# Kernel optimization log

Hardware: AMD Instinct MI355X
Metric: run time of the kernel (lower is better)

Reference implementation:

```python
import jax, jax.numpy as jnp
import numpy as np

N = 100000
E = 1600000
IN_C, HID, HEADS, OUT_C = 128, 32, 4, 32
NEG_SLOPE = 0.2


def gat_layer(x, edge_index, W, att_src, att_dst, bias, concat):
    """PyG-style GATConv: h = xW, per-edge attention, segment softmax over dst, scatter-add."""
    n = x.shape[0]
    H, C = att_src.shape
    h = (x @ W).reshape(n, H, C)                      # [N, H, C]
    src, dst = edge_index[0], edge_index[1]
    a_s = jnp.sum(h * att_src, axis=-1)               # [N, H]
    a_d = jnp.sum(h * att_dst, axis=-1)               # [N, H]
    e = jax.nn.leaky_relu(a_s[src] + a_d[dst], NEG_SLOPE)   # [E, H]
    # numerically stable segment softmax over incoming edges of each dst node
    m = jax.ops.segment_max(e, dst, num_segments=n)   # [N, H]
    ex = jnp.exp(e - m[dst])
    denom = jax.ops.segment_sum(ex, dst, num_segments=n)
    alpha = ex / denom[dst]                           # [E, H]
    msg = h[src] * alpha[:, :, None]                  # [E, H, C]
    out = jax.ops.segment_sum(msg, dst, num_segments=n)  # [N, H, C]
    out = out.reshape(n, H * C) if concat else out.mean(axis=1)
    return out + bias


def add_self_loops(edge_index, n):
    ar = jnp.arange(n, dtype=edge_index.dtype)
    loops = jnp.stack([ar, ar])
    return jnp.concatenate([edge_index, loops], axis=1)


def setup_inputs() -> dict:
    key = jax.random.key(0)
    ks = jax.random.split(key, 10)
    x = jax.random.normal(ks[0], (N, IN_C), dtype=jnp.float32)
    edge_index = jax.random.randint(ks[1], (2, E), 0, N, dtype=jnp.int64)
    s = 0.1
    W1 = jax.random.normal(ks[2], (IN_C, HEADS * HID), dtype=jnp.float32) * s
    att_src1 = jax.random.normal(ks[3], (HEADS, HID), dtype=jnp.float32) * s
    att_dst1 = jax.random.normal(ks[4], (HEADS, HID), dtype=jnp.float32) * s
    b1 = jnp.zeros((HEADS * HID,), dtype=jnp.float32)
    W2 = jax.random.normal(ks[5], (HEADS * HID, OUT_C), dtype=jnp.float32) * s
    att_src2 = jax.random.normal(ks[6], (1, OUT_C), dtype=jnp.float32) * s
    att_dst2 = jax.random.normal(ks[7], (1, OUT_C), dtype=jnp.float32) * s
    b2 = jnp.zeros((OUT_C,), dtype=jnp.float32)
    return {"x": x, "edge_index": edge_index,
            "W1": W1, "att_src1": att_src1, "att_dst1": att_dst1, "b1": b1,
            "W2": W2, "att_src2": att_src2, "att_dst2": att_dst2, "b2": b2}


def reference(x, edge_index, W1, att_src1, att_dst1, b1, W2, att_src2, att_dst2, b2):
    ei = add_self_loops(edge_index, x.shape[0])
    h = gat_layer(x, ei, W1, att_src1, att_dst1, b1, concat=True)
    h = jax.nn.elu(h)
    h = gat_layer(h, ei, W2, att_src2, att_dst2, b2, concat=False)
    return jax.nn.log_softmax(h, axis=1)
```

## Files before the change

### kernel.cpp

```cpp
#include <hip/hip_runtime.h>
#include <hip/hip_fp16.h>
#include <math.h>

#define IN_C   128
#define HEADS  4
#define F1     128
#define OUT_C  32
#define NEG    0.2f
#define SH     8
#define CHA    8192
#define SCB    4096

__device__ __forceinline__ unsigned short f2h(float f) {
    return __half_as_ushort(__float2half_rn(f));
}
__device__ __forceinline__ float h2f(unsigned short u) {
    return __half2float(__ushort_as_half(u));
}
__device__ __forceinline__ float hlo(unsigned u) { return h2f((unsigned short)(u & 0xffffu)); }
__device__ __forceinline__ float hhi(unsigned u) { return h2f((unsigned short)(u >> 16)); }
__device__ __forceinline__ unsigned pk2(float a, float b) {
    return (unsigned)f2h(a) | ((unsigned)f2h(b) << 16);
}
typedef _Float16 h2v __attribute__((ext_vector_type(2)));
__device__ __forceinline__ h2v u2h2(unsigned u) {
    h2v r; __builtin_memcpy(&r, &u, 4); return r;
}
__device__ __forceinline__ float dot2(unsigned a, unsigned b, float c) {
    return __builtin_amdgcn_fdot2(u2h2(a), u2h2(b), c, false);
}
#define PERM_LO 0x05040100u
#define PERM_HI 0x07060302u
__device__ __forceinline__ float pdot(unsigned b, unsigned a, unsigned sel, h2v pv, float c) {
    return __builtin_amdgcn_fdot2(u2h2(__builtin_amdgcn_perm(b, a, sel)), pv, c, false);
}

__global__ __launch_bounds__(256) void k_bhist(
    const int* __restrict__ ei, int* __restrict__ bmat, int E_, int n, int NB, int NC)
{
    __shared__ int h[512];
    int t = threadIdx.x, c = blockIdx.x;
    for (int i = t; i < NB; i += 256) h[i] = 0;
    __syncthreads();
    int e0 = c * CHA, e1 = min(e0 + CHA, E_ + n);
    for (int e = e0 + t; e < e1; e += 256) {
        int d = (e < E_) ? ei[E_ + e] : e - E_;
        atomicAdd(&h[d >> SH], 1);
    }
    __syncthreads();
    for (int i = t; i < NB; i += 256) bmat[i * NC + c] = h[i];
}

__global__ __launch_bounds__(256) void k_scanA(
    int* __restrict__ bmat, int* __restrict__ bsums, int M)
{
    __shared__ int sm[256];
    int t = threadIdx.x;
    int base = blockIdx.x * SCB + t * 16;
    int v[16];
    int s = 0;
    #pragma unroll
    for (int j = 0; j < 16; ++j) {
        int i = base + j;
        v[j] = (i < M) ? bmat[i] : 0;
        s += v[j];
    }
    sm[t] = s;
    __syncthreads();
    for (int off = 1; off < 256; off <<= 1) {
        int a = (t >= off) ? sm[t - off] : 0;
        __syncthreads();
        sm[t] += a;
        __syncthreads();
    }
    int excl = sm[t] - s;
    #pragma unroll
    for (int j = 0; j < 16; ++j) {
        int i = base + j;
        if (i < M) bmat[i] = excl;
        excl += v[j];
    }
    if (t == 255) bsums[blockIdx.x] = sm[255];
}

__global__ __launch_bounds__(256) void k_scanB(int* __restrict__ bsums, int NBLK)
{
    __shared__ int sm[256];
    int t = threadIdx.x;
    int v = (t < NBLK) ? bsums[t] : 0;
    sm[t] = v;
    __syncthreads();
    for (int off = 1; off < 256; off <<= 1) {
        int a = (t >= off) ? sm[t - off] : 0;
        __syncthreads();
        sm[t] += a;
        __syncthreads();
    }
    if (t < NBLK) bsums[t] = sm[t] - v;
}

__global__ __launch_bounds__(256) void k_scanC(
    int* __restrict__ bmat, const int* __restrict__ bsums, int M)
{
    int i = blockIdx.x * 256 + threadIdx.x;
    if (i < M) bmat[i] += bsums[i >> 12];
}

__global__ __launch_bounds__(256) void k_bscatter(
    const int* __restrict__ ei, const int* __restrict__ bmat,
    unsigned* __restrict__ recs, int E_, int n, int NB, int NC)
{
    __shared__ int cur[512];
    int t = threadIdx.x, c = blockIdx.x;
    for (int i = t; i < NB; i += 256) cur[i] = bmat[i * NC + c];
    __syncthreads();
    int e0 = c * CHA, e1 = min(e0 + CHA, E_ + n);
    for (int e = e0 + t; e < e1; e += 256) {
        int s, d;
        if (e < E_) { s = ei[e]; d = ei[E_ + e]; } else { s = d = e - E_; }
        int b = d >> SH;
        int p = atomicAdd(&cur[b], 1);
        recs[p] = ((unsigned)(d & ((1 << SH) - 1)) << 17) | (unsigned)s;
    }
}

__global__ __launch_bounds__(256) void k_bfill(
    const unsigned* __restrict__ recs, const int* __restrict__ bmat,
    int* __restrict__ row_off, int* __restrict__ csr, int n, int NB, int NC, int EE)
{
    __shared__ int deg[256];
    __shared__ int cur[256];
    int t = threadIdx.x, b = blockIdx.x;
    int r0 = bmat[b * NC];
    int r1 = (b + 1 < NB) ? bmat[(b + 1) * NC] : EE;
    deg[t] = 0;
    __syncthreads();
    for (int i = r0 + t; i < r1; i += 256)
        atomicAdd(&deg[recs[i] >> 17], 1);
    __syncthreads();
    int v = deg[t];
    for (int off = 1; off < 256; off <<= 1) {
        int a = (t >= off) ? deg[t - off] : 0;
        __syncthreads();
        deg[t] += a;
        __syncthreads();
    }
    int excl = deg[t] - v;
    int dst = (b << SH) + t;
    if (dst < n) row_off[dst] = r0 + excl;
    cur[t] = excl;
    if (b == NB - 1 && t == 0) row_off[n] = EE;
    __syncthreads();
    for (int i = r0 + t; i < r1; i += 256) {
        unsigned rec = recs[i];
        int dl = rec >> 17;
        int p = atomicAdd(&cur[dl], 1);
        csr[r0 + p] = (int)(rec & 0x1FFFFu);
    }
}

__global__ __launch_bounds__(256) void k_gemm1(
    const float* __restrict__ x, const float* __restrict__ W,
    const float* __restrict__ as_w, const float* __restrict__ ad_w,
    unsigned short* __restrict__ h1h, float* __restrict__ as1,
    float* __restrict__ ad1, int n)
{
    __shared__ unsigned Ws2[64 * 64];
    __shared__ unsigned xs2[64 * 64];
    int t = threadIdx.x;
    int half = blockIdx.x & 1;
    int n0 = (blockIdx.x >> 1) * 64;

    for (int i = t; i < 64 * 16; i += 256) {
        int k2 = i >> 4, c4 = (i & 15) * 4;
        const float* w0 = &W[(2 * k2) * 128 + half * 64 + c4];
        const float* w1 = &W[(2 * k2 + 1) * 128 + half * 64 + c4];
        float4 a = *(const float4*)w0;
        float4 b = *(const float4*)w1;
        uint4 p;
        p.x = pk2(a.x, b.x); p.y = pk2(a.y, b.y);
        p.z = pk2(a.z, b.z); p.w = pk2(a.w, b.w);
        *(uint4*)&Ws2[k2 * 64 + c4] = p;
    }
    for (int i = t; i < 64 * 32; i += 256) {
        int nl = i & 63, k4 = (i >> 6) * 4;
        int nn = n0 + nl;
        float4 v = (nn < n) ? *(const float4*)&x[(size_t)nn * 128 + k4]
                            : make_float4(0.f, 0.f, 0.f, 0.f);
        xs2[(k4 >> 1) * 64 + nl]       = pk2(v.x, v.y);
        xs2[((k4 >> 1) + 1) * 64 + nl] = pk2(v.z, v.w);
    }
    __syncthreads();

    int tx = t & 15, ty = t >> 4;
    float acc[4][4] = {};
    #pragma unroll 4
    for (int k2 = 0; k2 < 64; ++k2) {
        uint4 a = *(uint4*)&xs2[k2 * 64 + ty * 4];
        uint4 b = *(uint4*)&Ws2[k2 * 64 + tx * 4];
        unsigned av[4] = {a.x, a.y, a.z, a.w};
        unsigned bv[4] = {b.x, b.y, b.z, b.w};
        #pragma unroll
        for (int i = 0; i < 4; ++i)
            #pragma unroll
            for (int j = 0; j < 4; ++j)
                acc[i][j] = dot2(av[i], bv[j], acc[i][j]);
    }
    int cbase = half * 64 + tx * 4;
    float4 aws = *(const float4*)&as_w[cbase];
    float4 awd = *(const float4*)&ad_w[cbase];
    float sa[4], sd[4];
    #pragma unroll
    for (int i = 0; i < 4; ++i) {
        int nn = n0 + ty * 4 + i;
        sa[i] = acc[i][0]*aws.x + acc[i][1]*aws.y + acc[i][2]*aws.z + acc[i][3]*aws.w;
        sd[i] = acc[i][0]*awd.x + acc[i][1]*awd.y + acc[i][2]*awd.z + acc[i][3]*awd.w;
        if (nn < n) {
            ushort4 p;
            p.x = f2h(acc[i][0]); p.y = f2h(acc[i][1]);
            p.z = f2h(acc[i][2]); p.w = f2h(acc[i][3]);
            *(ushort4*)&h1h[(size_t)nn * 128 + cbase] = p;
        }
    }
    #pragma unroll
    for (int o = 1; o < 8; o <<= 1) {
        #pragma unroll
        for (int i = 0; i < 4; ++i) {
            sa[i] += __shfl_xor(sa[i], o);
            sd[i] += __shfl_xor(sd[i], o);
        }
    }
    if ((tx & 7) == 0) {
        int head = half * 2 + (tx >> 3);
        #pragma unroll
        for (int i = 0; i < 4; ++i) {
            int nn = n0 + ty * 4 + i;
            if (nn < n) {
                as1[(size_t)nn * 4 + head] = sa[i];
                ad1[(size_t)nn * 4 + head] = sd[i];
            }
        }
    }
}

__global__ __launch_bounds__(256) void k_gemm2(
    const float* __restrict__ z, const float* __restrict__ W,
    const float* __restrict__ as_w, const float* __restrict__ ad_w,
    unsigned short* __restrict__ h2h, float* __restrict__ as2,
    float* __restrict__ ad2, int n)
{
    __shared__ unsigned Ws2[64 * 32];
    __shared__ unsigned zs2[64 * 64];
    int t = threadIdx.x;
    int n0 = blockIdx.x * 64;

    for (int i = t; i < 64 * 8; i += 256) {
        int k2 = i >> 3, c4 = (i & 7) * 4;
        float4 a = *(const float4*)&W[(2 * k2) * 32 + c4];
        float4 b = *(const float4*)&W[(2 * k2 + 1) * 32 + c4];
        uint4 p;
        p.x = pk2(a.x, b.x); p.y = pk2(a.y, b.y);
        p.z = pk2(a.z, b.z); p.w = pk2(a.w, b.w);
        *(uint4*)&Ws2[k2 * 32 + c4] = p;
    }
    for (int i = t; i < 64 * 32; i += 256) {
        int nl = i & 63, k4 = (i >> 6) * 4;
        int nn = n0 + nl;
        float4 v = (nn < n) ? *(const float4*)&z[(size_t)nn * 128 + k4]
                            : make_float4(0.f, 0.f, 0.f, 0.f);
        zs2[(k4 >> 1) * 64 + nl]       = pk2(v.x, v.y);
        zs2[((k4 >> 1) + 1) * 64 + nl] = pk2(v.z, v.w);
    }
    __syncthreads();

    int tx = t & 7, ty = t >> 3;
    float acc[2][4] = {};
    #pragma unroll 4
    for (int k2 = 0; k2 < 64; ++k2) {
        uint2 a = *(uint2*)&zs2[k2 * 64 + ty * 2];
        uint4 b = *(uint4*)&Ws2[k2 * 32 + tx * 4];
        unsigned av[2] = {a.x, a.y};
        unsigned bv[4] = {b.x, b.y, b.z, b.w};
        #pragma unroll
        for (int i = 0; i < 2; ++i)
            #pragma unroll
            for (int j = 0; j < 4; ++j)
                acc[i][j] = dot2(av[i], bv[j], acc[i][j]);
    }
    float4 aws = *(const float4*)&as_w[tx * 4];
    float4 awd = *(const float4*)&ad_w[tx * 4];
    float sa[2], sd[2];
    #pragma unroll
    for (int i = 0; i < 2; ++i) {
        int nn = n0 + ty * 2 + i;
        sa[i] = acc[i][0]*aws.x + acc[i][1]*aws.y + acc[i][2]*aws.z + acc[i][3]*aws.w;
        sd[i] = acc[i][0]*awd.x + acc[i][1]*awd.y + acc[i][2]*awd.z + acc[i][3]*awd.w;
        if (nn < n) {
            ushort4 p;
            p.x = f2h(acc[i][0]); p.y = f2h(acc[i][1]);
            p.z = f2h(acc[i][2]); p.w = f2h(acc[i][3]);
            *(ushort4*)&h2h[(size_t)nn * 32 + tx * 4] = p;
        }
    }
    #pragma unroll
    for (int o = 1; o < 8; o <<= 1) {
        #pragma unroll
        for (int i = 0; i < 2; ++i) {
            sa[i] += __shfl_xor(sa[i], o);
            sd[i] += __shfl_xor(sd[i], o);
        }
    }
    if (tx == 0) {
        #pragma unroll
        for (int i = 0; i < 2; ++i) {
            int nn = n0 + ty * 2 + i;
            if (nn < n) { as2[nn] = sa[i]; ad2[nn] = sd[i]; }
        }
    }
}

__global__ __launch_bounds__(256) void k_gat1(
    const int* __restrict__ row_off, const int* __restrict__ csr,
    const float* __restrict__ as1, const float* __restrict__ ad1,
    const unsigned short* __restrict__ h1h, const float* __restrict__ b1,
    float* __restrict__ z, int n)
{
    int nb = threadIdx.x >> 4;
    int hl = threadIdx.x & 15;
    int node = blockIdx.x * 16 + nb;
    if (node >= n) return;
    __shared__ int            s_src[16][16];
    __shared__ unsigned short s_p16[16][4][16];
    int* ssrc = s_src[nb];
    unsigned short (*sp16)[16] = s_p16[nb];

    const char* h1b = (const char*)h1h;
    int chb  = hl << 4;
    int head = hl >> 2;

    float4 addv = *(const float4*)&ad1[(size_t)node * 4];
    int beg = row_off[node], end = row_off[node + 1];

    float sr0 = 0.f, sr1 = 0.f, sr2 = 0.f, sr3 = 0.f;
    float acc0 = 0.f, acc1 = 0.f, acc2 = 0.f, acc3 = 0.f;
    float acc4 = 0.f, acc5 = 0.f, acc6 = 0.f, acc7 = 0.f;

    for (int c = beg; c < end; c += 16) {
        int cnt = min(16, end - c);
        bool has = hl < cnt;
        float ls0 = 0.f, ls1 = 0.f, ls2 = 0.f, ls3 = 0.f;
        if (has) {
            int sA = csr[c + hl];
            ssrc[hl] = sA << 8;
            float4 av = *(const float4*)(as1 + ((unsigned)sA << 2));
            float v;
            v = av.x + addv.x; v = v > 0.f ? v : NEG * v; v = fminf(v, 10.f);
            unsigned short q0 = f2h(__expf(v));
            v = av.y + addv.y; v = v > 0.f ? v : NEG * v; v = fminf(v, 10.f);
            unsigned short q1 = f2h(__expf(v));
            v = av.z + addv.z; v = v > 0.f ? v : NEG * v; v = fminf(v, 10.f);
            unsigned short q2 = f2h(__expf(v));
            v = av.w + addv.w; v = v > 0.f ? v : NEG * v; v = fminf(v, 10.f);
            unsigned short q3 = f2h(__expf(v));
            sp16[0][hl] = q0; sp16[1][hl] = q1;
            sp16[2][hl] = q2; sp16[3][hl] = q3;
            ls0 = h2f(q0); ls1 = h2f(q1); ls2 = h2f(q2); ls3 = h2f(q3);
        }
        #pragma unroll
        for (int o = 8; o; o >>= 1) {
            ls0 += __shfl_xor(ls0, o);
            ls1 += __shfl_xor(ls1, o);
            ls2 += __shfl_xor(ls2, o);
            ls3 += __shfl_xor(ls3, o);
        }
        sr0 += ls0; sr1 += ls1; sr2 += ls2; sr3 += ls3;
        __threadfence_block();

        #define PAIR1(j) {                                                    \
            int2 oo = *(const int2*)&ssrc[j];                                 \
            unsigned pp = *(const unsigned*)&sp16[head][j];                   \
            uint4 A = *(const uint4*)(h1b + (unsigned)(oo.x + chb));          \
            uint4 B = *(const uint4*)(h1b + (unsigned)(oo.y + chb));          \
            h2v pv = u2h2(pp);                                                \
            acc0 = pdot(B.x, A.x, PERM_LO, pv, acc0);                         \
            acc1 = pdot(B.x, A.x, PERM_HI, pv, acc1);                         \
            acc2 = pdot(B.y, A.y, PERM_LO, pv, acc2);                         \
            acc3 = pdot(B.y, A.y, PERM_HI, pv, acc3);                         \
            acc4 = pdot(B.z, A.z, PERM_LO, pv, acc4);                         \
            acc5 = pdot(B.z, A.z, PERM_HI, pv, acc5);                         \
            acc6 = pdot(B.w, A.w, PERM_LO, pv, acc6);                         \
            acc7 = pdot(B.w, A.w, PERM_HI, pv, acc7);                         \
        }
        int jj = 0;
        for (; jj + 4 <= cnt; jj += 4) {
            PAIR1(jj);
            PAIR1(jj + 2);
        }
        if (jj + 2 <= cnt) {
            PAIR1(jj);
            jj += 2;
        }
        if (jj < cnt) {
            int o0 = ssrc[jj];
            float p = h2f(sp16[head][jj]);
            uint4 A = *(const uint4*)(h1b + (unsigned)(o0 + chb));
            acc0 = fmaf(p, hlo(A.x), acc0);
            acc1 = fmaf(p, hhi(A.x), acc1);
            acc2 = fmaf(p, hlo(A.y), acc2);
            acc3 = fmaf(p, hhi(A.y), acc3);
            acc4 = fmaf(p, hlo(A.z), acc4);
            acc5 = fmaf(p, hhi(A.z), acc5);
            acc6 = fmaf(p, hlo(A.w), acc6);
            acc7 = fmaf(p, hhi(A.w), acc7);
        }
        #undef PAIR1
    }
    float srh = head == 0 ? sr0 : head == 1 ? sr1 : head == 2 ? sr2 : sr3;
    float inv = 1.0f / srh;
    float4 bb0 = *(const float4*)&b1[hl * 8];
    float4 bb1 = *(const float4*)&b1[hl * 8 + 4];
    float v0 = acc0 * inv + bb0.x;
    float v1 = acc1 * inv + bb0.y;
    float v2 = acc2 * inv + bb0.z;
    float v3 = acc3 * inv + bb0.w;
    float v4 = acc4 * inv + bb1.x;
    float v5 = acc5 * inv + bb1.y;
    float v6 = acc6 * inv + bb1.z;
    float v7 = acc7 * inv + bb1.w;
    v0 = v0 > 0.f ? v0 : (__expf(v0) - 1.f);
    v1 = v1 > 0.f ? v1 : (__expf(v1) - 1.f);
    v2 = v2 > 0.f ? v2 : (__expf(v2) - 1.f);
    v3 = v3 > 0.f ? v3 : (__expf(v3) - 1.f);
    v4 = v4 > 0.f ? v4 : (__expf(v4) - 1.f);
    v5 = v5 > 0.f ? v5 : (__expf(v5) - 1.f);
    v6 = v6 > 0.f ? v6 : (__expf(v6) - 1.f);
    v7 = v7 > 0.f ? v7 : (__expf(v7) - 1.f);
    float* zr = &z[(size_t)node * F1 + hl * 8];
    *(float4*)zr       = make_float4(v0, v1, v2, v3);
    *(float4*)(zr + 4) = make_float4(v4, v5, v6, v7);
}

__global__ __launch_bounds__(256) void k_gat2(
    const int* __restrict__ row_off, const int* __restrict__ csr,
    const float* __restrict__ as2, const float* __restrict__ ad2,
    const unsigned short* __restrict__ h2h, const float* __restrict__ b2,
    float* __restrict__ y, int n)
{
    int nb = threadIdx.x >> 2;
    int hl = threadIdx.x & 3;
    int node = blockIdx.x * 64 + nb;
    if (node >= n) return;
    __shared__ int            s_src[64][34];
    __shared__ unsigned short s_p16[64][34];
    int* ssrc = s_src[nb];
    unsigned short* sp16 = s_p16[nb];

    const char* h2b = (const char*)h2h;
    int chb = hl << 4;

    float addv = ad2[node];
    int beg = row_off[node], end = row_off[node + 1];
    float sr = 0.f;
    float acc0 = 0.f, acc1 = 0.f, acc2 = 0.f, acc3 = 0.f;
    float acc4 = 0.f, acc5 = 0.f, acc6 = 0.f, acc7 = 0.f;

    for (int c = beg; c < end; c += 32) {
        int cnt = min(32, end - c);
        int e0 = hl << 3;
        float ls = 0.f;
        #pragma unroll
        for (int k = 0; k < 8; k += 2) {
            int e = e0 + k;
            if (e < cnt) {
                unsigned short qa, qb = 0;
                int sA = csr[c + e];
                ssrc[e] = sA << 6;
                float v = as2[(unsigned)sA] + addv;
                v = v > 0.f ? v : NEG * v;
                qa = f2h(__expf(fminf(v, 10.f)));
                if (e + 1 < cnt) {
                    int sB = csr[c + e + 1];
                    ssrc[e + 1] = sB << 6;
                    float w2 = as2[(unsigned)sB] + addv;
                    w2 = w2 > 0.f ? w2 : NEG * w2;
                    qb = f2h(__expf(fminf(w2, 10.f)));
                }
                *(unsigned*)&sp16[e] = (unsigned)qa | ((unsigned)qb << 16);
                ls += h2f(qa) + h2f(qb);
            }
        }
        ls += __shfl_xor(ls, 1);
        ls += __shfl_xor(ls, 2);
        sr += ls;
        __threadfence_block();

        #define PAIR2(j) {                                                    \
            int2 oo = *(const int2*)&ssrc[j];                                 \
            unsigned pp = *(const unsigned*)&sp16[j];                         \
            uint4 A = *(const uint4*)(h2b + (unsigned)(oo.x + chb));          \
            uint4 B = *(const uint4*)(h2b + (unsigned)(oo.y + chb));          \
            h2v pv = u2h2(pp);                                                \
            acc0 = pdot(B.x, A.x, PERM_LO, pv, acc0);                         \
            acc1 = pdot(B.x, A.x, PERM_HI, pv, acc1);                         \
            acc2 = pdot(B.y, A.y, PERM_LO, pv, acc2);                         \
            acc3 = pdot(B.y, A.y, PERM_HI, pv, acc3);                         \
            acc4 = pdot(B.z, A.z, PERM_LO, pv, acc4);                         \
            acc5 = pdot(B.z, A.z, PERM_HI, pv, acc5);                         \
            acc6 = pdot(B.w, A.w, PERM_LO, pv, acc6);                         \
            acc7 = pdot(B.w, A.w, PERM_HI, pv, acc7);                         \
        }
        int jj = 0;
        for (; jj + 4 <= cnt; jj += 4) {
            PAIR2(jj);
            PAIR2(jj + 2);
        }
        if (jj + 2 <= cnt) {
            PAIR2(jj);
            jj += 2;
        }
        if (jj < cnt) {
            int o0 = ssrc[jj];
            float p = h2f(sp16[jj]);
            uint4 A = *(const uint4*)(h2b + (unsigned)(o0 + chb));
            acc0 = fmaf(p, hlo(A.x), acc0);
            acc1 = fmaf(p, hhi(A.x), acc1);
            acc2 = fmaf(p, hlo(A.y), acc2);
            acc3 = fmaf(p, hhi(A.y), acc3);
            acc4 = fmaf(p, hlo(A.z), acc4);
            acc5 = fmaf(p, hhi(A.z), acc5);
            acc6 = fmaf(p, hlo(A.w), acc6);
            acc7 = fmaf(p, hhi(A.w), acc7);
        }
        #undef PAIR2
    }
    float inv = 1.0f / sr;
    float4 bb0 = *(const float4*)&b2[hl * 8];
    float4 bb1 = *(const float4*)&b2[hl * 8 + 4];
    float v0 = acc0 * inv + bb0.x;
    float v1 = acc1 * inv + bb0.y;
    float v2 = acc2 * inv + bb0.z;
    float v3 = acc3 * inv + bb0.w;
    float v4 = acc4 * inv + bb1.x;
    float v5 = acc5 * inv + bb1.y;
    float v6 = acc6 * inv + bb1.z;
    float v7 = acc7 * inv + bb1.w;
    float m = fmaxf(fmaxf(fmaxf(v0, v1), fmaxf(v2, v3)),
                    fmaxf(fmaxf(v4, v5), fmaxf(v6, v7)));
    m = fmaxf(m, __shfl_xor(m, 1));
    m = fmaxf(m, __shfl_xor(m, 2));
    float ss = __expf(v0 - m) + __expf(v1 - m) + __expf(v2 - m) + __expf(v3 - m)
             + __expf(v4 - m) + __expf(v5 - m) + __expf(v6 - m) + __expf(v7 - m);
    ss += __shfl_xor(ss, 1);
    ss += __shfl_xor(ss, 2);
    float lg = m + logf(ss);
    float* yr = &y[(size_t)node * OUT_C + hl * 8];
    *(float4*)yr       = make_float4(v0 - lg, v1 - lg, v2 - lg, v3 - lg);
    *(float4*)(yr + 4) = make_float4(v4 - lg, v5 - lg, v6 - lg, v7 - lg);
}

extern "C" void kernel_launch(void* const* d_in, const int* in_sizes, int n_in,
                              void* d_out, int out_size, void* d_ws, size_t ws_size,
                              hipStream_t stream) {
    const float* x    = (const float*)d_in[0];
    const int*   ei   = (const int*)d_in[1];
    const float* W1   = (const float*)d_in[2];
    const float* as1w = (const float*)d_in[3];
    const float* ad1w = (const float*)d_in[4];
    const float* b1   = (const float*)d_in[5];
    const float* W2   = (const float*)d_in[6];
    const float* as2w = (const float*)d_in[7];
    const float* ad2w = (const float*)d_in[8];
    const float* b2   = (const float*)d_in[9];
    float* out = (float*)d_out;

    int n  = in_sizes[0] / IN_C;
    int E_ = in_sizes[1] / 2;
    int EE = E_ + n;

    int NB = (n + (1 << SH) - 1) >> SH;
    int NC = (EE + CHA - 1) / CHA;
    int M  = NB * NC;
    int NBLK = (M + SCB - 1) / SCB;

    char* w = (char*)d_ws;
    size_t off = 0;
    auto take = [&](size_t elems) { void* p = w + off; off += ((elems * 4 + 255) & ~(size_t)255); return p; };
    int* bmat      = (int*)take((size_t)M);
    int* bsums     = (int*)take(256);
    unsigned* recs = (unsigned*)take((size_t)EE);
    int* row_off   = (int*)take((size_t)n + 1);
    int* csr       = (int*)take((size_t)EE);
    float* as1     = (float*)take((size_t)n * 4);
    float* ad1     = (float*)take((size_t)n * 4);
    unsigned short* h1h = (unsigned short*)take((size_t)n * 64);
    float* z       = (float*)take((size_t)n * 128);
    unsigned short* h2h = (unsigned short*)take((size_t)n * 16);
    float* as2     = (float*)take((size_t)n);
    float* ad2     = (float*)take((size_t)n);

    k_bhist   <<<NC, 256, 0, stream>>>(ei, bmat, E_, n, NB, NC);
    k_scanA   <<<NBLK, 256, 0, stream>>>(bmat, bsums, M);
    k_scanB   <<<1, 256, 0, stream>>>(bsums, NBLK);
    k_scanC   <<<(M + 255) / 256, 256, 0, stream>>>(bmat, bsums, M);
    k_bscatter<<<NC, 256, 0, stream>>>(ei, bmat, recs, E_, n, NB, NC);
    k_bfill   <<<NB, 256, 0, stream>>>(recs, bmat, row_off, csr, n, NB, NC, EE);

    int nt = (n + 63) / 64;
    k_gemm1<<<nt * 2, 256, 0, stream>>>(x, W1, as1w, ad1w, h1h, as1, ad1, n);
    int gG = (n + 15) / 16;
    k_gat1<<<gG, 256, 0, stream>>>(row_off, csr, as1, ad1, h1h, b1, z, n);

    k_gemm2<<<nt, 256, 0, stream>>>(z, W2, as2w, ad2w, h2h, as2, ad2, n);
    int gG2 = (n + 63) / 64;
    k_gat2<<<gG2, 256, 0, stream>>>(row_off, csr, as2, ad2, h2h, b2, out, n);
}
```

Measured before the change: 339.3 us.

## Fuse second-layer GEMM into GAT1 aggregation and fold scan fixup into consumers

The layer-2 linear transform and its attention-score dot products now run inside k_gat1. Each node's ELU output is packed to fp16 in shared memory and multiplied by a W2 tile held in LDS, so the 51 MB fp32 z intermediate is never written to or read back from global memory. The separate k_scanC pass is also removed: k_bscatter and k_bfill add the block offsets from bsums when they read bmat. The cost is that every gat1 block reloads and converts W2, plus extra LDS use that may lower occupancy.

```diff
diff --git a/kernel.cpp b/kernel.cpp
--- a/kernel.cpp
+++ b/kernel.cpp
@@ -99,20 +99,18 @@
     if (t < NBLK) bsums[t] = sm[t] - v;
 }
 
-__global__ __launch_bounds__(256) void k_scanC(
-    int* __restrict__ bmat, const int* __restrict__ bsums, int M)
-{
-    int i = blockIdx.x * 256 + threadIdx.x;
-    if (i < M) bmat[i] += bsums[i >> 12];
-}
 
 __global__ __launch_bounds__(256) void k_bscatter(
     const int* __restrict__ ei, const int* __restrict__ bmat,
-    unsigned* __restrict__ recs, int E_, int n, int NB, int NC)
+    const int* __restrict__ bsums, unsigned* __restrict__ recs,
+    int E_, int n, int NB, int NC)
 {
     __shared__ int cur[512];
     int t = threadIdx.x, c = blockIdx.x;
-    for (int i = t; i < NB; i += 256) cur[i] = bmat[i * NC + c];
+    for (int i = t; i < NB; i += 256) {
+        int m = i * NC + c;
+        cur[i] = bmat[m] + bsums[m >> 12];
+    }
     __syncthreads();
     int e0 = c * CHA, e1 = min(e0 + CHA, E_ + n);
     for (int e = e0 + t; e < e1; e += 256) {
@@ -126,13 +124,19 @@
 
 __global__ __launch_bounds__(256) void k_bfill(
     const unsigned* __restrict__ recs, const int* __restrict__ bmat,
-    int* __restrict__ row_off, int* __restrict__ csr, int n, int NB, int NC, int EE)
+    const int* __restrict__ bsums, int* __restrict__ row_off,
+    int* __restrict__ csr, int n, int NB, int NC, int EE)
 {
     __shared__ int deg[256];
     __shared__ int cur[256];
     int t = threadIdx.x, b = blockIdx.x;
-    int r0 = bmat[b * NC];
-    int r1 = (b + 1 < NB) ? bmat[(b + 1) * NC] : EE;
+    int m0 = b * NC;
+    int r0 = bmat[m0] + bsums[m0 >> 12];
+    int r1 = EE;
+    if (b + 1 < NB) {
+        int m1 = (b + 1) * NC;
+        r1 = bmat[m1] + bsums[m1 >> 12];
+    }
     deg[t] = 0;
     __syncthreads();
     for (int i = r0 + t; i < r1; i += 256)
@@ -243,201 +247,167 @@
     }
 }
 
-__global__ __launch_bounds__(256) void k_gemm2(
-    const float* __restrict__ z, const float* __restrict__ W,
-    const float* __restrict__ as_w, const float* __restrict__ ad_w,
-    unsigned short* __restrict__ h2h, float* __restrict__ as2,
-    float* __restrict__ ad2, int n)
-{
-    __shared__ unsigned Ws2[64 * 32];
-    __shared__ unsigned zs2[64 * 64];
-    int t = threadIdx.x;
-    int n0 = blockIdx.x * 64;
-
-    for (int i = t; i < 64 * 8; i += 256) {
-        int k2 = i >> 3, c4 = (i & 7) * 4;
-        float4 a = *(const float4*)&W[(2 * k2) * 32 + c4];
-        float4 b = *(const float4*)&W[(2 * k2 + 1) * 32 + c4];
-        uint4 p;
-        p.x = pk2(a.x, b.x); p.y = pk2(a.y, b.y);
-        p.z = pk2(a.z, b.z); p.w = pk2(a.w, b.w);
-        *(uint4*)&Ws2[k2 * 32 + c4] = p;
-    }
-    for (int i = t; i < 64 * 32; i += 256) {
-        int nl = i & 63, k4 = (i >> 6) * 4;
-        int nn = n0 + nl;
-        float4 v = (nn < n) ? *(const float4*)&z[(size_t)nn * 128 + k4]
-                            : make_float4(0.f, 0.f, 0.f, 0.f);
-        zs2[(k4 >> 1) * 64 + nl]       = pk2(v.x, v.y);
-        zs2[((k4 >> 1) + 1) * 64 + nl] = pk2(v.z, v.w);
-    }
-    __syncthreads();
-
-    int tx = t & 7, ty = t >> 3;
-    float acc[2][4] = {};
-    #pragma unroll 4
-    for (int k2 = 0; k2 < 64; ++k2) {
-        uint2 a = *(uint2*)&zs2[k2 * 64 + ty * 2];
-        uint4 b = *(uint4*)&Ws2[k2 * 32 + tx * 4];
-        unsigned av[2] = {a.x, a.y};
-        unsigned bv[4] = {b.x, b.y, b.z, b.w};
-        #pragma unroll
-        for (int i = 0; i < 2; ++i)
-            #pragma unroll
-            for (int j = 0; j < 4; ++j)
-                acc[i][j] = dot2(av[i], bv[j], acc[i][j]);
-    }
-    float4 aws = *(const float4*)&as_w[tx * 4];
-    float4 awd = *(const float4*)&ad_w[tx * 4];
-    float sa[2], sd[2];
-    #pragma unroll
-    for (int i = 0; i < 2; ++i) {
-        int nn = n0 + ty * 2 + i;
-        sa[i] = acc[i][0]*aws.x + acc[i][1]*aws.y + acc[i][2]*aws.z + acc[i][3]*aws.w;
-        sd[i] = acc[i][0]*awd.x + acc[i][1]*awd.y + acc[i][2]*awd.z + acc[i][3]*awd.w;
-        if (nn < n) {
-            ushort4 p;
-            p.x = f2h(acc[i][0]); p.y = f2h(acc[i][1]);
-            p.z = f2h(acc[i][2]); p.w = f2h(acc[i][3]);
-            *(ushort4*)&h2h[(size_t)nn * 32 + tx * 4] = p;
-        }
-    }
-    #pragma unroll
-    for (int o = 1; o < 8; o <<= 1) {
-        #pragma unroll
-        for (int i = 0; i < 2; ++i) {
-            sa[i] += __shfl_xor(sa[i], o);
-            sd[i] += __shfl_xor(sd[i], o);
-        }
-    }
-    if (tx == 0) {
-        #pragma unroll
-        for (int i = 0; i < 2; ++i) {
-            int nn = n0 + ty * 2 + i;
-            if (nn < n) { as2[nn] = sa[i]; ad2[nn] = sd[i]; }
-        }
-    }
-}
-
 __global__ __launch_bounds__(256) void k_gat1(
     const int* __restrict__ row_off, const int* __restrict__ csr,
     const float* __restrict__ as1, const float* __restrict__ ad1,
     const unsigned short* __restrict__ h1h, const float* __restrict__ b1,
-    float* __restrict__ z, int n)
-{
-    int nb = threadIdx.x >> 4;
-    int hl = threadIdx.x & 15;
-    int node = blockIdx.x * 16 + nb;
-    if (node >= n) return;
+    const float* __restrict__ W2, const float* __restrict__ as2w,
+    const float* __restrict__ ad2w, unsigned short* __restrict__ h2h,
+    float* __restrict__ as2, float* __restrict__ ad2, int n)
+{
     __shared__ int            s_src[16][16];
     __shared__ unsigned short s_p16[16][4][16];
-    int* ssrc = s_src[nb];
-    unsigned short (*sp16)[16] = s_p16[nb];
-
-    const char* h1b = (const char*)h1h;
-    int chb  = hl << 4;
-    int head = hl >> 2;
-
-    float4 addv = *(const float4*)&ad1[(size_t)node * 4];
-    int beg = row_off[node], end = row_off[node + 1];
-
-    float sr0 = 0.f, sr1 = 0.f, sr2 = 0.f, sr3 = 0.f;
-    float acc0 = 0.f, acc1 = 0.f, acc2 = 0.f, acc3 = 0.f;
-    float acc4 = 0.f, acc5 = 0.f, acc6 = 0.f, acc7 = 0.f;
-
-    for (int c = beg; c < end; c += 16) {
-        int cnt = min(16, end - c);
-        bool has = hl < cnt;
-        float ls0 = 0.f, ls1 = 0.f, ls2 = 0.f, ls3 = 0.f;
-        if (has) {
-            int sA = csr[c + hl];
-            ssrc[hl] = sA << 8;
-            float4 av = *(const float4*)(as1 + ((unsigned)sA << 2));
-            float v;
-            v = av.x + addv.x; v = v > 0.f ? v : NEG * v; v = fminf(v, 10.f);
-            unsigned short q0 = f2h(__expf(v));
-            v = av.y + addv.y; v = v > 0.f ? v : NEG * v; v = fminf(v, 10.f);
-            unsigned short q1 = f2h(__expf(v));
-            v = av.z + addv.z; v = v > 0.f ? v : NEG * v; v = fminf(v, 10.f);
-            unsigned short q2 = f2h(__expf(v));
-            v = av.w + addv.w; v = v > 0.f ? v : NEG * v; v = fminf(v, 10.f);
-            unsigned short q3 = f2h(__expf(v));
-            sp16[0][hl] = q0; sp16[1][hl] = q1;
-            sp16[2][hl] = q2; sp16[3][hl] = q3;
-            ls0 = h2f(q0); ls1 = h2f(q1); ls2 = h2f(q2); ls3 = h2f(q3);
-        }
+    __shared__ unsigned       W2s[64 * 32];
+    __shared__ unsigned       zs[16][66];
+    int t = threadIdx.x;
+
+    for (int i = t; i < 64 * 8; i += 256) {
+        int k2 = i >> 3, c4 = (i & 7) * 4;
+        float4 a = *(const float4*)&W2[(2 * k2) * 32 + c4];
+        float4 b = *(const float4*)&W2[(2 * k2 + 1) * 32 + c4];
+        uint4 p;
+        p.x = pk2(a.x, b.x); p.y = pk2(a.y, b.y);
+        p.z = pk2(a.z, b.z); p.w = pk2(a.w, b.w);
+        *(uint4*)&W2s[k2 * 32 + c4] = p;
+    }
+    __syncthreads();
+
+    int nb = t >> 4;
+    int hl = t & 15;
+    int node = blockIdx.x * 16 + nb;
+    if (node < n) {
+        int* ssrc = s_src[nb];
+        unsigned short (*sp16)[16] = s_p16[nb];
+
+        const char* h1b = (const char*)h1h;
+        int chb  = hl << 4;
+        int head = hl >> 2;
+
+        float4 addv = *(const float4*)&ad1[(size_t)node * 4];
+        int beg = row_off[node], end = row_off[node + 1];
+
+        float sr0 = 0.f, sr1 = 0.f, sr2 = 0.f, sr3 = 0.f;
+        float acc0 = 0.f, acc1 = 0.f, acc2 = 0.f, acc3 = 0.f;
+        float acc4 = 0.f, acc5 = 0.f, acc6 = 0.f, acc7 = 0.f;
+
+        for (int c = beg; c < end; c += 16) {
+            int cnt = min(16, end - c);
+            bool has = hl < cnt;
+            float ls0 = 0.f, ls1 = 0.f, ls2 = 0.f, ls3 = 0.f;
+            if (has) {
+                int sA = csr[c + hl];
+                ssrc[hl] = sA << 8;
+                float4 av = *(const float4*)(as1 + ((unsigned)sA << 2));
+                float v;
+                v = av.x + addv.x; v = v > 0.f ? v : NEG * v; v = fminf(v, 10.f);
+                unsigned short q0 = f2h(__expf(v));
+                v = av.y + addv.y; v = v > 0.f ? v : NEG * v; v = fminf(v, 10.f);
+                unsigned short q1 = f2h(__expf(v));
+                v = av.z + addv.z; v = v > 0.f ? v : NEG * v; v = fminf(v, 10.f);
+                unsigned short q2 = f2h(__expf(v));
+                v = av.w + addv.w; v = v > 0.f ? v : NEG * v; v = fminf(v, 10.f);
+                unsigned short q3 = f2h(__expf(v));
+                sp16[0][hl] = q0; sp16[1][hl] = q1;
+                sp16[2][hl] = q2; sp16[3][hl] = q3;
+                ls0 = h2f(q0); ls1 = h2f(q1); ls2 = h2f(q2); ls3 = h2f(q3);
+            }
+            #pragma unroll
+            for (int o = 8; o; o >>= 1) {
+                ls0 += __shfl_xor(ls0, o);
+                ls1 += __shfl_xor(ls1, o);
+                ls2 += __shfl_xor(ls2, o);
+                ls3 += __shfl_xor(ls3, o);
+            }
+            sr0 += ls0; sr1 += ls1; sr2 += ls2; sr3 += ls3;
+            __threadfence_block();
+
+            #define PAIR1(j) {                                                    \
+                int2 oo = *(const int2*)&ssrc[j];                                 \
+                unsigned pp = *(const unsigned*)&sp16[head][j];                   \
+                uint4 A = *(const uint4*)(h1b + (unsigned)(oo.x + chb));          \
+                uint4 B = *(const uint4*)(h1b + (unsigned)(oo.y + chb));          \
+                h2v pv = u2h2(pp);                                                \
+                acc0 = pdot(B.x, A.x, PERM_LO, pv, acc0);                         \
+                acc1 = pdot(B.x, A.x, PERM_HI, pv, acc1);                         \
+                acc2 = pdot(B.y, A.y, PERM_LO, pv, acc2);                         \
+                acc3 = pdot(B.y, A.y, PERM_HI, pv, acc3);                         \
+                acc4 = pdot(B.z, A.z, PERM_LO, pv, acc4);                         \
+                acc5 = pdot(B.z, A.z, PERM_HI, pv, acc5);                         \
+                acc6 = pdot(B.w, A.w, PERM_LO, pv, acc6);                         \
+                acc7 = pdot(B.w, A.w, PERM_HI, pv, acc7);                         \
+            }
+            int jj = 0;
+            for (; jj + 4 <= cnt; jj += 4) {
+                PAIR1(jj);
+                PAIR1(jj + 2);
+            }
+            if (jj + 2 <= cnt) {
+                PAIR1(jj);
+                jj += 2;
+            }
+            if (jj < cnt) {
+                int o0 = ssrc[jj];
+                float p = h2f(sp16[head][jj]);
+                uint4 A = *(const uint4*)(h1b + (unsigned)(o0 + chb));
+                acc0 = fmaf(p, hlo(A.x), acc0);
+                acc1 = fmaf(p, hhi(A.x), acc1);
+                acc2 = fmaf(p, hlo(A.y), acc2);
+                acc3 = fmaf(p, hhi(A.y), acc3);
+                acc4 = fmaf(p, hlo(A.z), acc4);
+                acc5 = fmaf(p, hhi(A.z), acc5);
+                acc6 = fmaf(p, hlo(A.w), acc6);
+                acc7 = fmaf(p, hhi(A.w), acc7);
+            }
+            #undef PAIR1
+        }
+        float srh = head == 0 ? sr0 : head == 1 ? sr1 : head == 2 ? sr2 : sr3;
+        float inv = 1.0f / srh;
+        float4 bb0 = *(const float4*)&b1[hl * 8];
+        float4 bb1 = *(const float4*)&b1[hl * 8 + 4];
+        float v0 = acc0 * inv + bb0.x;
+        float v1 = acc1 * inv + bb0.y;
+        float v2 = acc2 * inv + bb0.z;
+        float v3 = acc3 * inv + bb0.w;
+        float v4 = acc4 * inv + bb1.x;
+        float v5 = acc5 * inv + bb1.y;
+        float v6 = acc6 * inv + bb1.z;
+        float v7 = acc7 * inv + bb1.w;
+        v0 = v0 > 0.f ? v0 : (__expf(v0) - 1.f);
+        v1 = v1 > 0.f ? v1 : (__expf(v1) - 1.f);
+        v2 = v2 > 0.f ? v2 : (__expf(v2) - 1.f);
+        v3 = v3 > 0.f ? v3 : (__expf(v3) - 1.f);
+        v4 = v4 > 0.f ? v4 : (__expf(v4) - 1.f);
+        v5 = v5 > 0.f ? v5 : (__expf(v5) - 1.f);
+        v6 = v6 > 0.f ? v6 : (__expf(v6) - 1.f);
+        v7 = v7 > 0.f ? v7 : (__expf(v7) - 1.f);
+
+        unsigned* zrow = zs[nb];
+        zrow[hl * 4 + 0] = pk2(v0, v1);
+        zrow[hl * 4 + 1] = pk2(v2, v3);
+        zrow[hl * 4 + 2] = pk2(v4, v5);
+        zrow[hl * 4 + 3] = pk2(v6, v7);
+        __threadfence_block();
+        int c0 = hl * 2;
+        float a0 = 0.f, a1 = 0.f;
+        #pragma unroll 8
+        for (int k2 = 0; k2 < 64; ++k2) {
+            unsigned zp = zrow[k2];
+            uint2 wp = *(const uint2*)&W2s[k2 * 32 + c0];
+            a0 = dot2(zp, wp.x, a0);
+            a1 = dot2(zp, wp.y, a1);
+        }
+        *(unsigned*)&h2h[(size_t)node * 32 + c0] = pk2(a0, a1);
+        float2 asw = *(const float2*)&as2w[c0];
+        float2 adw = *(const float2*)&ad2w[c0];
+        float sa = a0 * asw.x + a1 * asw.y;
+        float sd = a0 * adw.x + a1 * adw.y;
         #pragma unroll
         for (int o = 8; o; o >>= 1) {
-            ls0 += __shfl_xor(ls0, o);
-            ls1 += __shfl_xor(ls1, o);
-            ls2 += __shfl_xor(ls2, o);
-            ls3 += __shfl_xor(ls3, o);
-        }
-        sr0 += ls0; sr1 += ls1; sr2 += ls2; sr3 += ls3;
-        __threadfence_block();
-
-        #define PAIR1(j) {                                                    \
-            int2 oo = *(const int2*)&ssrc[j];                                 \
-            unsigned pp = *(const unsigned*)&sp16[head][j];                   \
-            uint4 A = *(const uint4*)(h1b + (unsigned)(oo.x + chb));          \
-            uint4 B = *(const uint4*)(h1b + (unsigned)(oo.y + chb));          \
-            h2v pv = u2h2(pp);                                                \
-            acc0 = pdot(B.x, A.x, PERM_LO, pv, acc0);                         \
-            acc1 = pdot(B.x, A.x, PERM_HI, pv, acc1);                         \
-            acc2 = pdot(B.y, A.y, PERM_LO, pv, acc2);                         \
-            acc3 = pdot(B.y, A.y, PERM_HI, pv, acc3);                         \
-            acc4 = pdot(B.z, A.z, PERM_LO, pv, acc4);                         \
-            acc5 = pdot(B.z, A.z, PERM_HI, pv, acc5);                         \
-            acc6 = pdot(B.w, A.w, PERM_LO, pv, acc6);                         \
-            acc7 = pdot(B.w, A.w, PERM_HI, pv, acc7);                         \
-        }
-        int jj = 0;
-        for (; jj + 4 <= cnt; jj += 4) {
-            PAIR1(jj);
-            PAIR1(jj + 2);
-        }
-        if (jj + 2 <= cnt) {
-            PAIR1(jj);
-            jj += 2;
-        }
-        if (jj < cnt) {
-            int o0 = ssrc[jj];
-            float p = h2f(sp16[head][jj]);
-            uint4 A = *(const uint4*)(h1b + (unsigned)(o0 + chb));
-            acc0 = fmaf(p, hlo(A.x), acc0);
-            acc1 = fmaf(p, hhi(A.x), acc1);
-            acc2 = fmaf(p, hlo(A.y), acc2);
-            acc3 = fmaf(p, hhi(A.y), acc3);
-            acc4 = fmaf(p, hlo(A.z), acc4);
-            acc5 = fmaf(p, hhi(A.z), acc5);
-            acc6 = fmaf(p, hlo(A.w), acc6);
-            acc7 = fmaf(p, hhi(A.w), acc7);
-        }
-        #undef PAIR1
-    }
-    float srh = head == 0 ? sr0 : head == 1 ? sr1 : head == 2 ? sr2 : sr3;
-    float inv = 1.0f / srh;
-    float4 bb0 = *(const float4*)&b1[hl * 8];
-    float4 bb1 = *(const float4*)&b1[hl * 8 + 4];
-    float v0 = acc0 * inv + bb0.x;
-    float v1 = acc1 * inv + bb0.y;
-    float v2 = acc2 * inv + bb0.z;
-    float v3 = acc3 * inv + bb0.w;
-    float v4 = acc4 * inv + bb1.x;
-    float v5 = acc5 * inv + bb1.y;
-    float v6 = acc6 * inv + bb1.z;
-    float v7 = acc7 * inv + bb1.w;
-    v0 = v0 > 0.f ? v0 : (__expf(v0) - 1.f);
-    v1 = v1 > 0.f ? v1 : (__expf(v1) - 1.f);
-    v2 = v2 > 0.f ? v2 : (__expf(v2) - 1.f);
-    v3 = v3 > 0.f ? v3 : (__expf(v3) - 1.f);
-    v4 = v4 > 0.f ? v4 : (__expf(v4) - 1.f);
-    v5 = v5 > 0.f ? v5 : (__expf(v5) - 1.f);
-    v6 = v6 > 0.f ? v6 : (__expf(v6) - 1.f);
-    v7 = v7 > 0.f ? v7 : (__expf(v7) - 1.f);
-    float* zr = &z[(size_t)node * F1 + hl * 8];
-    *(float4*)zr       = make_float4(v0, v1, v2, v3);
-    *(float4*)(zr + 4) = make_float4(v4, v5, v6, v7);
+            sa += __shfl_xor(sa, o);
+            sd += __shfl_xor(sd, o);
+        }
+        if (hl == 0) { as2[node] = sa; ad2[node] = sd; }
+    }
 }
 
 __global__ __launch_bounds__(256) void k_gat2(
@@ -593,7 +563,6 @@
     float* as1     = (float*)take((size_t)n * 4);
     float* ad1     = (float*)take((size_t)n * 4);
     unsigned short* h1h = (unsigned short*)take((size_t)n * 64);
-    float* z       = (float*)take((size_t)n * 128);
     unsigned short* h2h = (unsigned short*)take((size_t)n * 16);
     float* as2     = (float*)take((size_t)n);
     float* ad2     = (float*)take((size_t)n);
@@ -601,16 +570,16 @@
     k_bhist   <<<NC, 256, 0, stream>>>(ei, bmat, E_, n, NB, NC);
     k_scanA   <<<NBLK, 256, 0, stream>>>(bmat, bsums, M);
     k_scanB   <<<1, 256, 0, stream>>>(bsums, NBLK);
-    k_scanC   <<<(M + 255) / 256, 256, 0, stream>>>(bmat, bsums, M);
-    k_bscatter<<<NC, 256, 0, stream>>>(ei, bmat, recs, E_, n, NB, NC);
-    k_bfill   <<<NB, 256, 0, stream>>>(recs, bmat, row_off, csr, n, NB, NC, EE);
+    k_bscatter<<<NC, 256, 0, stream>>>(ei, bmat, bsums, recs, E_, n, NB, NC);
+    k_bfill   <<<NB, 256, 0, stream>>>(recs, bmat, bsums, row_off, csr, n, NB, NC, EE);
 
     int nt = (n + 63) / 64;
     k_gemm1<<<nt * 2, 256, 0, stream>>>(x, W1, as1w, ad1w, h1h, as1, ad1, n);
+
     int gG = (n + 15) / 16;
-    k_gat1<<<gG, 256, 0, stream>>>(row_off, csr, as1, ad1, h1h, b1, z, n);
-
-    k_gemm2<<<nt, 256, 0, stream>>>(z, W2, as2w, ad2w, h2h, as2, ad2, n);
+    k_gat1<<<gG, 256, 0, stream>>>(row_off, csr, as1, ad1, h1h, b1,
+                                   W2, as2w, ad2w, h2h, as2, ad2, n);
+
     int gG2 = (n + 63) / 64;
     k_gat2<<<gG2, 256, 0, stream>>>(row_off, csr, as2, ad2, h2h, b2, out, n);
 }
```

After: 303.4 us. 1.12x faster.
